# Performance work log

Hardware: AMD Instinct MI355X
Metric: run time of the kernel (lower is better)

## Reference

```python
import jax, jax.numpy as jnp
import numpy as np

L, B, CIN, H, W = 32, 4, 3, 16, 16
D, HEADS, DK, DEPTH = 64, 4, 16, 2
EPS = 1e-5
BN_INV = float(1.0 / np.sqrt(1.0 + EPS))  # eval-mode BatchNorm with default stats/affine


def conv2d(x, w, b=None, pad=1, groups=1):
    y = jax.lax.conv_general_dilated(
        x, w, window_strides=(1, 1), padding=[(pad, pad), (pad, pad)],
        dimension_numbers=('NCHW', 'OIHW', 'NCHW'), feature_group_count=groups)
    if b is not None:
        y = y + b[None, :, None, None]
    return y


def layer_norm(x, w, b):
    # LayerNorm over last 3 dims [D,H,W] of (L,B,D,H,W)
    mu = jnp.mean(x, axis=(-3, -2, -1), keepdims=True)
    var = jnp.var(x, axis=(-3, -2, -1), keepdims=True)
    return (x - mu) * jax.lax.rsqrt(var + EPS) * w + b


def pos_table():
    pos = jnp.arange(L, dtype=jnp.float32)
    exp = (2.0 * (jnp.arange(D) // 2).astype(jnp.float32)) / D
    angle = pos[:, None] / jnp.power(10000.0, exp)[None, :]  # (L, D)
    # source applies sin to even POSITIONS and cos to odd POSITIONS (table[0::2]=sin)
    tab = jnp.where((jnp.arange(L) % 2 == 0)[:, None], jnp.sin(angle), jnp.cos(angle))
    return tab[:, None, :, None, None]  # (L,1,D,1,1) broadcast over B,H,W


def reference(x, gw1, gb1, gw2, gb2, gw3, gb3, gw4, gb4,
              conv1_w, conv1_b, conv2_w, conv2_b, wq, wk, wv, w0,
              ln1_w, ln1_b, ln2_w, ln2_b, ff_w1, ff_b1, ff_w2, ff_b2):
    lrelu = lambda v: jax.nn.leaky_relu(v, 0.01)
    h = x.reshape(L * B, CIN, H, W)
    for w_, b_ in ((gw1, gb1), (gw2, gb2), (gw3, gb3), (gw4, gb4)):
        h = lrelu(conv2d(h, w_, b_) * BN_INV)
    xlb = h.reshape(L, B, D, H, W) + pos_table()

    for i in range(DEPTH):
        # ---- multi-head conv attention (dec=True) ----
        y = layer_norm(xlb, ln1_w[i], ln1_b[i])
        xa = jnp.transpose(y, (1, 2, 3, 4, 0))  # (B,D,H,W,L)
        # conv1 is a 1x1 conv == pointwise linear over channels, per head
        qkv = jnp.einsum('bchwl,noc->bnohwl', xa, conv1_w[i]) \
            + conv1_b[i][None, :, :, None, None, None]  # (B,HEADS,3D,H,W,L)
        q, k, v = jnp.split(qkv, 3, axis=2)  # each (B,HEADS,D,H,W,L)
        q = jnp.einsum('bnchwl,nck->bnkhwl', q, wq[i])  # (B,HEADS,DK,H,W,L)
        k = jnp.einsum('bnchwl,nck->bnkhwl', k, wk[i])
        v = jnp.einsum('bnchwl,nck->bnkhwl', v, wv[i])

        def head_conv(t):
            # 5x5 conv per head (no bias): conv2(Q_i + K_j) = conv_w(Q)_i + conv_w(K)_j + bias
            z = jnp.transpose(t, (0, 5, 1, 2, 3, 4)).reshape(B * L, HEADS * DK, H, W)
            z = conv2d(z, conv2_w[i].reshape(HEADS * DK, DK, 5, 5), None, pad=2, groups=HEADS)
            return jnp.transpose(z.reshape(B, L, HEADS, DK, H, W), (0, 2, 3, 4, 5, 1))

        cq = head_conv(q)
        ck = head_conv(k)
        logits = cq[..., :, None] + ck[..., None, :] \
            + conv2_b[i][None, :, :, None, None, None, None]  # (B,HEADS,DK,H,W,Lq,Lk)
        a = jax.nn.softmax(logits, axis=-1)
        vout = jnp.einsum('bnkhwij,bnkhwj->bnkhwi', a, v)   # (B,HEADS,DK,H,W,L)
        vcat = vout.reshape(B, D, H, W, L)                  # concat heads on channel dim
        attn = jnp.einsum('bchwl,co->bohwl', vcat, w0[i])
        xlb = xlb + jnp.transpose(attn, (4, 0, 1, 2, 3))

        # ---- feed-forward over the TIME dimension (Linear on L) ----
        y = layer_norm(xlb, ln2_w[i], ln2_b[i])
        xp = jnp.transpose(y, (1, 2, 3, 4, 0))  # (B,D,H,W,L)
        h1 = lrelu(jnp.einsum('bchwl,ml->bchwm', xp, ff_w1[i]) + ff_b1[i])
        ff = jnp.einsum('bchwm,lm->bchwl', h1, ff_w2[i]) + ff_b2[i]
        xlb = xlb + jnp.transpose(ff, (4, 0, 1, 2, 3))
    return xlb


def setup_inputs() -> dict:
    key = jax.random.key(0)
    specs = {
        'x': (L, B, CIN, H, W),
        'gw1': (4, 3, 3, 3), 'gb1': (4,), 'gw2': (6, 4, 3, 3), 'gb2': (6,),
        'gw3': (8, 6, 3, 3), 'gb3': (8,), 'gw4': (64, 8, 3, 3), 'gb4': (64,),
        'conv1_w': (DEPTH, HEADS, 3 * D, D), 'conv1_b': (DEPTH, HEADS, 3 * D),
        'conv2_w': (DEPTH, HEADS, DK, DK, 5, 5), 'conv2_b': (DEPTH, HEADS, DK),
        'wq': (DEPTH, HEADS, D, DK), 'wk': (DEPTH, HEADS, D, DK), 'wv': (DEPTH, HEADS, D, DK),
        'w0': (DEPTH, D, D),
        'ln1_w': (DEPTH, D, H, W), 'ln1_b': (DEPTH, D, H, W),
        'ln2_w': (DEPTH, D, H, W), 'ln2_b': (DEPTH, D, H, W),
        'ff_w1': (DEPTH, 4 * L, L), 'ff_b1': (DEPTH, 4 * L),
        'ff_w2': (DEPTH, L, 4 * L), 'ff_b2': (DEPTH, L),
    }
    out = {}
    for idx, (name, shape) in enumerate(specs.items()):
        g = jax.random.normal(jax.random.fold_in(key, idx), shape, dtype=jnp.float32)
        if name == 'x':
            out[name] = g
        elif name in ('ln1_w', 'ln2_w'):
            out[name] = 1.0 + 0.05 * g
        else:
            out[name] = 0.05 * g
    return out
```

## Files before the change

### kernel.cpp

```cpp
#include <hip/hip_runtime.h>
#include <math.h>

#define LL 32
#define BB 4
#define DD 64
#define NH 4
#define DKK 16
#define BN_INV 0.9999950000374997f

__device__ __forceinline__ float lrelu(float v){ return v > 0.f ? v : 0.01f*v; }

__global__ void k_eff(const float* __restrict__ c1w, const float* __restrict__ c1b,
                      const float* __restrict__ wk, const float* __restrict__ wv,
                      float* __restrict__ A, float* __restrict__ bf){
  int tid = blockIdx.x*256 + threadIdx.x;
  int k = tid & 15, d = (tid>>4)&63, n=(tid>>10)&3, t=(tid>>12)&1, i=tid>>13;
  const float* wsel = (t ? wv : wk) + (i*NH+n)*64*16;
  const float* cw   = c1w + ((i*NH+n)*192 + (t+1)*64)*64;
  float acc = 0.f;
  for(int c=0;c<64;++c) acc += cw[c*64+d]*wsel[c*16+k];
  A[tid] = acc;
  if(d==0){
    const float* cb = c1b + (i*NH+n)*192 + (t+1)*64;
    float ba=0.f;
    for(int c=0;c<64;++c) ba += cb[c]*wsel[c*16+k];
    bf[((i*2+t)*4+n)*16+k] = ba;
  }
}

__global__ void k_pos(float* __restrict__ pos){
  int tid = blockIdx.x*256 + threadIdx.x;
  int d = tid & 63, l = tid >> 6;
  float ex = (float)(d>>1) / 32.0f;
  float angle = (float)l * powf(10000.0f, -ex);
  pos[tid] = (l & 1) ? cosf(angle) : sinf(angle);
}

__global__ void k_wT(const float* __restrict__ w2, float* __restrict__ wT){
  int tid = blockIdx.x*256 + threadIdx.x;
  int k = tid & 15; int rest = tid >> 4;
  int tap = rest % 25; int rest2 = rest / 25;
  int c = rest2 & 15; int dn = rest2 >> 4;
  wT[tid] = w2[((dn*16 + k)*16 + c)*25 + tap];
}

__global__ void k_wT3(const float* __restrict__ gw4, float* __restrict__ wT3){
  int tid = blockIdx.x*256 + threadIdx.x;
  if(tid >= 4608) return;
  int co = tid & 63, ct = tid >> 6;
  wT3[ct*64 + co] = gw4[co*72 + ct];
}

__global__ void k_w2T(const float* __restrict__ w2, float* __restrict__ w2T){
  int tid = blockIdx.x*256 + threadIdx.x;
  int l = tid & 31; int m = (tid>>5)&127; int dep = tid>>12;
  w2T[tid] = w2[dep*4096 + l*128 + m];
}

__global__ __launch_bounds__(256) void k_front(const float* __restrict__ x,
    const float* __restrict__ gw1, const float* __restrict__ gb1,
    const float* __restrict__ gw2, const float* __restrict__ gb2,
    const float* __restrict__ gw3, const float* __restrict__ gb3,
    float* __restrict__ out8){
  __shared__ float sh[4212];
  float* T0 = sh; float* T1 = sh + 972; float* T2 = sh + 2268;
  int f = blockIdx.x, t = threadIdx.x;
  int h = t>>4, w = t&15;
  for(int j=t;j<4212;j+=256) sh[j]=0.f;
  __syncthreads();
  for(int ci=0;ci<3;++ci) T0[ci*324 + (h+1)*18 + (w+1)] = x[f*768 + ci*256 + t];
  __syncthreads();
  for(int co=0;co<4;++co){
    float acc = gb1[co];
    for(int ci=0;ci<3;++ci){
      const float* tb = T0 + ci*324 + h*18 + w;
      const float* wb = gw1 + co*27 + ci*9;
      #pragma unroll
      for(int dy=0;dy<3;++dy)
        #pragma unroll
        for(int dx=0;dx<3;++dx) acc += tb[dy*18+dx]*wb[dy*3+dx];
    }
    T1[co*324 + (h+1)*18 + (w+1)] = lrelu(acc*BN_INV);
  }
  __syncthreads();
  for(int co=0;co<6;++co){
    float acc = gb2[co];
    for(int ci=0;ci<4;++ci){
      const float* tb = T1 + ci*324 + h*18 + w;
      const float* wb = gw2 + co*36 + ci*9;
      #pragma unroll
      for(int dy=0;dy<3;++dy)
        #pragma unroll
        for(int dx=0;dx<3;++dx) acc += tb[dy*18+dx]*wb[dy*3+dx];
    }
    T2[co*324 + (h+1)*18 + (w+1)] = lrelu(acc*BN_INV);
  }
  __syncthreads();
  for(int co=0;co<8;++co){
    float acc = gb3[co];
    for(int ci=0;ci<6;++ci){
      const float* tb = T2 + ci*324 + h*18 + w;
      const float* wb = gw3 + co*54 + ci*9;
      #pragma unroll
      for(int dy=0;dy<3;++dy)
        #pragma unroll
        for(int dx=0;dx<3;++dx) acc += tb[dy*18+dx]*wb[dy*3+dx];
    }
    out8[f*2048 + co*256 + t] = lrelu(acc*BN_INV);
  }
}

__global__ __launch_bounds__(256) void k_conv3_l4(const float* __restrict__ in8,
    const float* __restrict__ wT3, const float* __restrict__ gb4,
    const float* __restrict__ pos, float* __restrict__ out){
  __shared__ float tile[8*324];
  __shared__ float wsl[1152];
  int blk = blockIdx.x; int g = blk & 3; int f = blk >> 2;
  int t = threadIdx.x; int h = t>>4, w = t&15;
  for(int j=t;j<2592;j+=256) tile[j]=0.f;
  for(int j=t;j<1152;j+=256){
    int ct = j>>4, c16 = j&15;
    wsl[j] = wT3[ct*64 + g*16 + c16];
  }
  __syncthreads();
  for(int ci=0;ci<8;++ci) tile[ci*324 + (h+1)*18 + (w+1)] = in8[f*2048 + ci*256 + t];
  __syncthreads();
  float acc[16];
  #pragma unroll
  for(int q=0;q<16;++q) acc[q] = gb4[g*16+q];
  for(int ci=0;ci<8;++ci){
    const float* tb = tile + ci*324 + h*18 + w;
    #pragma unroll
    for(int dy=0;dy<3;++dy){
      #pragma unroll
      for(int dx=0;dx<3;++dx){
        float v = tb[dy*18+dx];
        const float* wp = wsl + (ci*9+dy*3+dx)*16;
        float4 wa = *(const float4*)(wp);
        float4 wb = *(const float4*)(wp+4);
        float4 wc = *(const float4*)(wp+8);
        float4 wd = *(const float4*)(wp+12);
        acc[0]+=v*wa.x; acc[1]+=v*wa.y; acc[2]+=v*wa.z; acc[3]+=v*wa.w;
        acc[4]+=v*wb.x; acc[5]+=v*wb.y; acc[6]+=v*wb.z; acc[7]+=v*wb.w;
        acc[8]+=v*wc.x; acc[9]+=v*wc.y; acc[10]+=v*wc.z; acc[11]+=v*wc.w;
        acc[12]+=v*wd.x; acc[13]+=v*wd.y; acc[14]+=v*wd.z; acc[15]+=v*wd.w;
      }
    }
  }
  int l = f >> 2;
  #pragma unroll
  for(int q=0;q<16;++q){
    float r = lrelu(acc[q]*BN_INV) + pos[l*64 + g*16 + q];
    out[f*16384 + (g*16+q)*256 + t] = r;
  }
}

__global__ __launch_bounds__(1024) void k_ln(const float* __restrict__ x,
                     const float* __restrict__ w, const float* __restrict__ b,
                     float* __restrict__ y){
  int g = blockIdx.x, t = threadIdx.x;
  const float4* xb = (const float4*)(x + g*16384);
  float4 xv[4];
  float s=0.f, s2=0.f;
  #pragma unroll
  for(int j=0;j<4;++j){
    float4 v = xb[t + j*1024];
    xv[j] = v;
    s  += v.x + v.y + v.z + v.w;
    s2 += v.x*v.x + v.y*v.y + v.z*v.z + v.w*v.w;
  }
  __shared__ float ls[1024], ls2[1024];
  ls[t]=s; ls2[t]=s2; __syncthreads();
  for(int off=512;off>0;off>>=1){
    if(t<off){ ls[t]+=ls[t+off]; ls2[t]+=ls2[t+off]; }
    __syncthreads();
  }
  float mu  = ls[0]*(1.0f/16384.f);
  float var = ls2[0]*(1.0f/16384.f) - mu*mu;
  float rinv = rsqrtf(var + 1e-5f);
  const float4* wb = (const float4*)w;
  const float4* bb = (const float4*)b;
  float4* yb = (float4*)(y + g*16384);
  #pragma unroll
  for(int j=0;j<4;++j){
    int e = t + j*1024;
    float4 v = xv[j], wv = wb[e], bv = bb[e], o;
    o.x = (v.x-mu)*rinv*wv.x + bv.x;
    o.y = (v.y-mu)*rinv*wv.y + bv.y;
    o.z = (v.z-mu)*rinv*wv.z + bv.z;
    o.w = (v.w-mu)*rinv*wv.w + bv.w;
    yb[e] = o;
  }
}

__global__ __launch_bounds__(256) void k_kv(const float* __restrict__ y,
                     const float* __restrict__ A, const float* __restrict__ bf,
                     float* __restrict__ K, float* __restrict__ V, int dep){
  int blk = blockIdx.x;
  int n = blk & 3; int lb = blk >> 2;
  int t = threadIdx.x;
  const float* yb  = y + lb*16384 + t;
  const float* akb = A + ((dep*2+0)*4+n)*1024;
  const float* avb = A + ((dep*2+1)*4+n)*1024;
  float kacc[16], vacc[16];
  #pragma unroll
  for(int q=0;q<16;++q){
    kacc[q] = bf[((dep*2+0)*4+n)*16+q];
    vacc[q] = bf[((dep*2+1)*4+n)*16+q];
  }
  for(int d=0;d<64;++d){
    float yv = yb[d*256];
    const float* ak = akb + d*16;
    const float* av = avb + d*16;
    #pragma unroll
    for(int q=0;q<16;++q){ kacc[q] += yv*ak[q]; vacc[q] += yv*av[q]; }
  }
  int l = lb >> 2, b = lb & 3;
  int base = ((b*32+l)*4+n)*4096 + t;
  #pragma unroll
  for(int q=0;q<16;++q){ K[base + q*256] = kacc[q]; V[base + q*256] = vacc[q]; }
}

__global__ __launch_bounds__(256) void k_conv5(const float* __restrict__ K,
                       const float* __restrict__ wT, float* __restrict__ CK, int dep){
  __shared__ float tile[16*400];
  int blk = blockIdx.x;
  int khalf = blk & 1; int fh = blk >> 1; int n = fh & 3;
  int t = threadIdx.x;
  const float* kb = K + fh*4096;
  for(int j=t;j<6400;j+=256) tile[j]=0.f;
  __syncthreads();
  int h = t>>4, w = t&15;
  for(int c=0;c<16;++c) tile[c*400 + (h+2)*20 + (w+2)] = kb[c*256+t];
  __syncthreads();
  const float* wb = wT + (dep*4+n)*6400 + khalf*8;
  float acc[8] = {0.f,0.f,0.f,0.f,0.f,0.f,0.f,0.f};
  for(int c=0;c<16;++c){
    const float* tb = tile + c*400 + h*20 + w;
    const float* wc = wb + c*400;
    #pragma unroll
    for(int dy=0;dy<5;++dy){
      #pragma unroll
      for(int dx=0;dx<5;++dx){
        float v = tb[dy*20+dx];
        const float* wp = wc + (dy*5+dx)*16;
        float4 wa = *(const float4*)(wp);
        float4 wbv = *(const float4*)(wp+4);
        acc[0]+=v*wa.x; acc[1]+=v*wa.y; acc[2]+=v*wa.z; acc[3]+=v*wa.w;
        acc[4]+=v*wbv.x; acc[5]+=v*wbv.y; acc[6]+=v*wbv.z; acc[7]+=v*wbv.w;
      }
    }
  }
  float* ob = CK + fh*4096 + khalf*8*256;
  #pragma unroll
  for(int q=0;q<8;++q) ob[q*256+t] = acc[q];
}

__global__ void k_soft(const float* __restrict__ CK, const float* __restrict__ V,
                       float* __restrict__ vout){
  int idx = blockIdx.x*256 + threadIdx.x;
  int p = idx&255; int k=(idx>>8)&15; int n=(idx>>12)&3; int b=idx>>14;
  int base = (b*128 + n)*4096 + k*256 + p;
  float e[32]; float m = -1e30f;
  for(int l=0;l<32;++l){ float v = CK[base + l*16384]; e[l]=v; m = fmaxf(m,v); }
  float s = 0.f;
  for(int l=0;l<32;++l){ e[l] = expf(e[l]-m); s += e[l]; }
  float inv = 1.f/s, acc = 0.f;
  for(int l=0;l<32;++l) acc += e[l]*V[base + l*16384];
  vout[((b*4+n)*16+k)*256+p] = acc*inv;
}

__global__ void k_w0res(const float* __restrict__ vout, const float* __restrict__ w0,
                        float* __restrict__ xlb, int dep){
  int idx = blockIdx.x*256 + threadIdx.x;
  int p = idx&255; int o=(idx>>8)&63; int b=idx>>14;
  const float* vb = vout + b*64*256 + p;
  const float* wb = w0 + dep*4096 + o;
  float acc = 0.f;
  for(int c=0;c<64;++c) acc += vb[c*256]*wb[c*64];
  for(int l=0;l<32;++l) xlb[((l*4+b)*64+o)*256 + p] += acc;
}

__global__ __launch_bounds__(256) void k_ff(const float* __restrict__ y,
                     const float* __restrict__ w1, const float* __restrict__ b1,
                     const float* __restrict__ w2T, const float* __restrict__ b2,
                     float* __restrict__ xlb, int dep){
  __shared__ float pfa[4*2048];
  int t = threadIdx.x;
  int lane = t & 63;
  int w = __builtin_amdgcn_readfirstlane(t >> 6);
  int blk = blockIdx.x;
  int elem = blk*64 + lane;
  float yv[32];
  #pragma unroll
  for(int l=0;l<32;++l) yv[l] = y[elem + l*65536];
  float fa[32];
  if(w==0){
    #pragma unroll
    for(int l=0;l<32;++l) fa[l] = b2[dep*32+l];
  } else {
    #pragma unroll
    for(int l=0;l<32;++l) fa[l] = 0.f;
  }
  const float* w1b  = w1  + dep*4096 + w*1024;
  const float* w2Tb = w2T + dep*4096 + w*1024;
  const float* b1b  = b1  + dep*128  + w*32;
  #pragma unroll 4
  for(int mm=0;mm<32;++mm){
    float s0=0.f,s1=0.f,s2=0.f,s3=0.f;
    #pragma unroll
    for(int l=0;l<32;l+=4){
      s0 += yv[l+0]*w1b[mm*32+l+0];
      s1 += yv[l+1]*w1b[mm*32+l+1];
      s2 += yv[l+2]*w1b[mm*32+l+2];
      s3 += yv[l+3]*w1b[mm*32+l+3];
    }
    float s = lrelu(((s0+s1)+(s2+s3)) + b1b[mm]);
    #pragma unroll
    for(int l=0;l<32;++l) fa[l] += s*w2Tb[mm*32+l];
  }
  #pragma unroll
  for(int l=0;l<32;++l) pfa[w*2048 + l*64 + lane] = fa[l];
  __syncthreads();
  #pragma unroll
  for(int j=0;j<8;++j){
    int pi = t + j*256;
    float sum = pfa[pi] + pfa[pi+2048] + pfa[pi+4096] + pfa[pi+6144];
    int l = pi >> 6, ln2 = pi & 63;
    xlb[blk*64 + ln2 + l*65536] += sum;
  }
}

extern "C" void kernel_launch(void* const* d_in, const int* in_sizes, int n_in,
                              void* d_out, int out_size, void* d_ws, size_t ws_size,
                              hipStream_t stream) {
  const float* x       = (const float*)d_in[0];
  const float* gw1     = (const float*)d_in[1];
  const float* gb1     = (const float*)d_in[2];
  const float* gw2     = (const float*)d_in[3];
  const float* gb2     = (const float*)d_in[4];
  const float* gw3     = (const float*)d_in[5];
  const float* gb3     = (const float*)d_in[6];
  const float* gw4     = (const float*)d_in[7];
  const float* gb4     = (const float*)d_in[8];
  const float* conv1_w = (const float*)d_in[9];
  const float* conv1_b = (const float*)d_in[10];
  const float* conv2_w = (const float*)d_in[11];
  const float* wk      = (const float*)d_in[14];
  const float* wv      = (const float*)d_in[15];
  const float* w0      = (const float*)d_in[16];
  const float* ln1_w   = (const float*)d_in[17];
  const float* ln1_b   = (const float*)d_in[18];
  const float* ln2_w   = (const float*)d_in[19];
  const float* ln2_b   = (const float*)d_in[20];
  const float* ff_w1   = (const float*)d_in[21];
  const float* ff_b1   = (const float*)d_in[22];
  const float* ff_w2   = (const float*)d_in[23];
  const float* ff_b2   = (const float*)d_in[24];

  float* out = (float*)d_out;
  float* ws  = (float*)d_ws;
  float* Y    = ws;
  float* K    = ws + 2097152;
  float* CK   = ws + 4194304;
  float* V    = ws + 6291456;
  float* vout = ws + 8388608;
  float* A    = ws + 8454144;
  float* bf   = ws + 8470528;
  float* pos  = ws + 8470784;
  float* wT   = ws + 8472832;
  float* wT3  = ws + 8524032;
  float* w2T  = ws + 8528640;

  k_eff<<<64, 256, 0, stream>>>(conv1_w, conv1_b, wk, wv, A, bf);
  k_pos<<<8, 256, 0, stream>>>(pos);
  k_wT <<<200, 256, 0, stream>>>(conv2_w, wT);
  k_wT3<<<18, 256, 0, stream>>>(gw4, wT3);
  k_w2T<<<32, 256, 0, stream>>>(ff_w2, w2T);

  k_front   <<<128, 256, 0, stream>>>(x, gw1, gb1, gw2, gb2, gw3, gb3, K);
  k_conv3_l4<<<512, 256, 0, stream>>>(K, wT3, gb4, pos, out);

  for(int dep=0; dep<2; ++dep){
    k_ln   <<<128, 1024, 0, stream>>>(out, ln1_w + dep*16384, ln1_b + dep*16384, Y);
    k_kv   <<<512,  256, 0, stream>>>(Y, A, bf, K, V, dep);
    k_conv5<<<1024, 256, 0, stream>>>(K, wT, CK, dep);
    k_soft <<<256,  256, 0, stream>>>(CK, V, vout);
    k_w0res<<<256,  256, 0, stream>>>(vout, w0, out, dep);
    k_ln   <<<128, 1024, 0, stream>>>(out, ln2_w + dep*16384, ln2_b + dep*16384, Y);
    k_ff   <<<1024, 256, 0, stream>>>(Y, ff_w1, ff_b1, w2T, ff_b2, out, dep);
  }
}
```

Measured before the change: 326.3 us.

## Fuse LayerNorm apply into consumers and merge weight-prep kernels

Replaces the LayerNorm kernel, which wrote a full normalized tensor Y, with a stats-only kernel that stores mean and inverse std per frame. The normalization is then applied on the fly inside k_kv and k_ff, and k_ff reuses its loaded x values for the residual instead of re-reading and accumulating. The five small weight-prep kernels are merged into one launch. This removes a full write and read of Y per LayerNorm and several launches, at the cost of redundant normalization arithmetic: k_kv recomputes it across the 4 heads, and k_ff recomputes it across its 4 waves.

```diff
diff --git a/kernel.cpp b/kernel.cpp
--- a/kernel.cpp
+++ b/kernel.cpp
@@ -10,51 +10,49 @@
 
 __device__ __forceinline__ float lrelu(float v){ return v > 0.f ? v : 0.01f*v; }
 
-__global__ void k_eff(const float* __restrict__ c1w, const float* __restrict__ c1b,
-                      const float* __restrict__ wk, const float* __restrict__ wv,
-                      float* __restrict__ A, float* __restrict__ bf){
-  int tid = blockIdx.x*256 + threadIdx.x;
-  int k = tid & 15, d = (tid>>4)&63, n=(tid>>10)&3, t=(tid>>12)&1, i=tid>>13;
-  const float* wsel = (t ? wv : wk) + (i*NH+n)*64*16;
-  const float* cw   = c1w + ((i*NH+n)*192 + (t+1)*64)*64;
-  float acc = 0.f;
-  for(int c=0;c<64;++c) acc += cw[c*64+d]*wsel[c*16+k];
-  A[tid] = acc;
-  if(d==0){
-    const float* cb = c1b + (i*NH+n)*192 + (t+1)*64;
-    float ba=0.f;
-    for(int c=0;c<64;++c) ba += cb[c]*wsel[c*16+k];
-    bf[((i*2+t)*4+n)*16+k] = ba;
-  }
-}
-
-__global__ void k_pos(float* __restrict__ pos){
-  int tid = blockIdx.x*256 + threadIdx.x;
-  int d = tid & 63, l = tid >> 6;
-  float ex = (float)(d>>1) / 32.0f;
-  float angle = (float)l * powf(10000.0f, -ex);
-  pos[tid] = (l & 1) ? cosf(angle) : sinf(angle);
-}
-
-__global__ void k_wT(const float* __restrict__ w2, float* __restrict__ wT){
-  int tid = blockIdx.x*256 + threadIdx.x;
-  int k = tid & 15; int rest = tid >> 4;
-  int tap = rest % 25; int rest2 = rest / 25;
-  int c = rest2 & 15; int dn = rest2 >> 4;
-  wT[tid] = w2[((dn*16 + k)*16 + c)*25 + tap];
-}
-
-__global__ void k_wT3(const float* __restrict__ gw4, float* __restrict__ wT3){
-  int tid = blockIdx.x*256 + threadIdx.x;
-  if(tid >= 4608) return;
-  int co = tid & 63, ct = tid >> 6;
-  wT3[ct*64 + co] = gw4[co*72 + ct];
-}
-
-__global__ void k_w2T(const float* __restrict__ w2, float* __restrict__ w2T){
-  int tid = blockIdx.x*256 + threadIdx.x;
-  int l = tid & 31; int m = (tid>>5)&127; int dep = tid>>12;
-  w2T[tid] = w2[dep*4096 + l*128 + m];
+__global__ __launch_bounds__(256) void k_prep(
+    const float* __restrict__ c1w, const float* __restrict__ c1b,
+    const float* __restrict__ wk,  const float* __restrict__ wv,
+    const float* __restrict__ w2,  const float* __restrict__ gw4,
+    const float* __restrict__ ffw2,
+    float* __restrict__ A, float* __restrict__ bf, float* __restrict__ pos,
+    float* __restrict__ wT, float* __restrict__ wT3, float* __restrict__ w2T){
+  int blk = blockIdx.x, t = threadIdx.x;
+  if(blk < 64){
+    int tid = blk*256 + t;
+    int k = tid & 15, d = (tid>>4)&63, n=(tid>>10)&3, tt=(tid>>12)&1, i=tid>>13;
+    const float* wsel = (tt ? wv : wk) + (i*NH+n)*64*16;
+    const float* cw   = c1w + ((i*NH+n)*192 + (tt+1)*64)*64;
+    float acc = 0.f;
+    for(int c=0;c<64;++c) acc += cw[c*64+d]*wsel[c*16+k];
+    A[tid] = acc;
+    if(d==0){
+      const float* cb = c1b + (i*NH+n)*192 + (tt+1)*64;
+      float ba=0.f;
+      for(int c=0;c<64;++c) ba += cb[c]*wsel[c*16+k];
+      bf[((i*2+tt)*4+n)*16+k] = ba;
+    }
+  } else if(blk < 72){
+    int tid = (blk-64)*256 + t;
+    int d = tid & 63, l = tid >> 6;
+    float ex = (float)(d>>1) / 32.0f;
+    float angle = (float)l * powf(10000.0f, -ex);
+    pos[tid] = (l & 1) ? cosf(angle) : sinf(angle);
+  } else if(blk < 272){
+    int tid = (blk-72)*256 + t;
+    int k = tid & 15; int rest = tid >> 4;
+    int tap = rest % 25; int rest2 = rest / 25;
+    int c = rest2 & 15; int dn = rest2 >> 4;
+    wT[tid] = w2[((dn*16 + k)*16 + c)*25 + tap];
+  } else if(blk < 290){
+    int tid = (blk-272)*256 + t;
+    int co = tid & 63, ct = tid >> 6;
+    wT3[ct*64 + co] = gw4[co*72 + ct];
+  } else {
+    int tid = (blk-290)*256 + t;
+    int l = tid & 31; int m = (tid>>5)&127; int dep = tid>>12;
+    w2T[tid] = ffw2[dep*4096 + l*128 + m];
+  }
 }
 
 __global__ __launch_bounds__(256) void k_front(const float* __restrict__ x,
@@ -155,17 +153,14 @@
   }
 }
 
-__global__ __launch_bounds__(1024) void k_ln(const float* __restrict__ x,
-                     const float* __restrict__ w, const float* __restrict__ b,
-                     float* __restrict__ y){
+__global__ __launch_bounds__(1024) void k_stats(const float* __restrict__ x,
+                                                float* __restrict__ stats){
   int g = blockIdx.x, t = threadIdx.x;
   const float4* xb = (const float4*)(x + g*16384);
-  float4 xv[4];
   float s=0.f, s2=0.f;
   #pragma unroll
   for(int j=0;j<4;++j){
     float4 v = xb[t + j*1024];
-    xv[j] = v;
     s  += v.x + v.y + v.z + v.w;
     s2 += v.x*v.x + v.y*v.y + v.z*v.z + v.w*v.w;
   }
@@ -175,31 +170,26 @@
     if(t<off){ ls[t]+=ls[t+off]; ls2[t]+=ls2[t+off]; }
     __syncthreads();
   }
-  float mu  = ls[0]*(1.0f/16384.f);
-  float var = ls2[0]*(1.0f/16384.f) - mu*mu;
-  float rinv = rsqrtf(var + 1e-5f);
-  const float4* wb = (const float4*)w;
-  const float4* bb = (const float4*)b;
-  float4* yb = (float4*)(y + g*16384);
-  #pragma unroll
-  for(int j=0;j<4;++j){
-    int e = t + j*1024;
-    float4 v = xv[j], wv = wb[e], bv = bb[e], o;
-    o.x = (v.x-mu)*rinv*wv.x + bv.x;
-    o.y = (v.y-mu)*rinv*wv.y + bv.y;
-    o.z = (v.z-mu)*rinv*wv.z + bv.z;
-    o.w = (v.w-mu)*rinv*wv.w + bv.w;
-    yb[e] = o;
-  }
-}
-
-__global__ __launch_bounds__(256) void k_kv(const float* __restrict__ y,
+  if(t==0){
+    float mu  = ls[0]*(1.0f/16384.f);
+    float var = ls2[0]*(1.0f/16384.f) - mu*mu;
+    stats[g*2]   = mu;
+    stats[g*2+1] = rsqrtf(var + 1e-5f);
+  }
+}
+
+__global__ __launch_bounds__(256) void k_kv(const float* __restrict__ x,
+                     const float* __restrict__ lnw, const float* __restrict__ lnb,
+                     const float* __restrict__ stats,
                      const float* __restrict__ A, const float* __restrict__ bf,
                      float* __restrict__ K, float* __restrict__ V, int dep){
   int blk = blockIdx.x;
   int n = blk & 3; int lb = blk >> 2;
   int t = threadIdx.x;
-  const float* yb  = y + lb*16384 + t;
+  float mu = stats[lb*2], ri = stats[lb*2+1];
+  const float* xb  = x   + lb*16384 + t;
+  const float* wbp = lnw + t;
+  const float* bbp = lnb + t;
   const float* akb = A + ((dep*2+0)*4+n)*1024;
   const float* avb = A + ((dep*2+1)*4+n)*1024;
   float kacc[16], vacc[16];
@@ -209,7 +199,7 @@
     vacc[q] = bf[((dep*2+1)*4+n)*16+q];
   }
   for(int d=0;d<64;++d){
-    float yv = yb[d*256];
+    float yv = (xb[d*256]-mu)*ri*wbp[d*256] + bbp[d*256];
     const float* ak = akb + d*16;
     const float* av = avb + d*16;
     #pragma unroll
@@ -281,19 +271,31 @@
   for(int l=0;l<32;++l) xlb[((l*4+b)*64+o)*256 + p] += acc;
 }
 
-__global__ __launch_bounds__(256) void k_ff(const float* __restrict__ y,
+__global__ __launch_bounds__(256) void k_ff(float* __restrict__ xlb,
+                     const float* __restrict__ lnw, const float* __restrict__ lnb,
+                     const float* __restrict__ stats,
                      const float* __restrict__ w1, const float* __restrict__ b1,
                      const float* __restrict__ w2T, const float* __restrict__ b2,
-                     float* __restrict__ xlb, int dep){
+                     int dep){
   __shared__ float pfa[4*2048];
   int t = threadIdx.x;
   int lane = t & 63;
   int w = __builtin_amdgcn_readfirstlane(t >> 6);
   int blk = blockIdx.x;
   int elem = blk*64 + lane;
-  float yv[32];
-  #pragma unroll
-  for(int l=0;l<32;++l) yv[l] = y[elem + l*65536];
+  int b = elem >> 14;
+  int e = elem & 16383;
+  float lw  = lnw[e];
+  float lbv = lnb[e];
+  float xv[32], yv[32];
+  #pragma unroll
+  for(int l=0;l<32;++l) xv[l] = xlb[elem + l*65536];
+  #pragma unroll
+  for(int l=0;l<32;++l){
+    float mu = stats[(l*4+b)*2];
+    float ri = stats[(l*4+b)*2+1];
+    yv[l] = (xv[l]-mu)*ri*lw + lbv;
+  }
   float fa[32];
   if(w==0){
     #pragma unroll
@@ -326,8 +328,8 @@
   for(int j=0;j<8;++j){
     int pi = t + j*256;
     float sum = pfa[pi] + pfa[pi+2048] + pfa[pi+4096] + pfa[pi+6144];
-    int l = pi >> 6, ln2 = pi & 63;
-    xlb[blk*64 + ln2 + l*65536] += sum;
+    int l = pi >> 6;
+    xlb[blk*64 + lane + l*65536] = xv[l] + sum;
   }
 }
 
@@ -360,34 +362,33 @@
 
   float* out = (float*)d_out;
   float* ws  = (float*)d_ws;
-  float* Y    = ws;
-  float* K    = ws + 2097152;
-  float* CK   = ws + 4194304;
-  float* V    = ws + 6291456;
-  float* vout = ws + 8388608;
-  float* A    = ws + 8454144;
-  float* bf   = ws + 8470528;
-  float* pos  = ws + 8470784;
-  float* wT   = ws + 8472832;
-  float* wT3  = ws + 8524032;
-  float* w2T  = ws + 8528640;
-
-  k_eff<<<64, 256, 0, stream>>>(conv1_w, conv1_b, wk, wv, A, bf);
-  k_pos<<<8, 256, 0, stream>>>(pos);
-  k_wT <<<200, 256, 0, stream>>>(conv2_w, wT);
-  k_wT3<<<18, 256, 0, stream>>>(gw4, wT3);
-  k_w2T<<<32, 256, 0, stream>>>(ff_w2, w2T);
+  float* K     = ws;
+  float* CK    = ws + 2097152;
+  float* V     = ws + 4194304;
+  float* vout  = ws + 6291456;
+  float* A     = ws + 6356992;
+  float* bf    = ws + 6373376;
+  float* pos   = ws + 6373632;
+  float* wT    = ws + 6375680;
+  float* wT3   = ws + 6426880;
+  float* w2T   = ws + 6431488;
+  float* stats = ws + 6439680;
+
+  k_prep<<<322, 256, 0, stream>>>(conv1_w, conv1_b, wk, wv, conv2_w, gw4, ff_w2,
+                                  A, bf, pos, wT, wT3, w2T);
 
   k_front   <<<128, 256, 0, stream>>>(x, gw1, gb1, gw2, gb2, gw3, gb3, K);
   k_conv3_l4<<<512, 256, 0, stream>>>(K, wT3, gb4, pos, out);
 
   for(int dep=0; dep<2; ++dep){
-    k_ln   <<<128, 1024, 0, stream>>>(out, ln1_w + dep*16384, ln1_b + dep*16384, Y);
-    k_kv   <<<512,  256, 0, stream>>>(Y, A, bf, K, V, dep);
+    k_stats<<<128, 1024, 0, stream>>>(out, stats);
+    k_kv   <<<512,  256, 0, stream>>>(out, ln1_w + dep*16384, ln1_b + dep*16384,
+                                      stats, A, bf, K, V, dep);
     k_conv5<<<1024, 256, 0, stream>>>(K, wT, CK, dep);
     k_soft <<<256,  256, 0, stream>>>(CK, V, vout);
     k_w0res<<<256,  256, 0, stream>>>(vout, w0, out, dep);
-    k_ln   <<<128, 1024, 0, stream>>>(out, ln2_w + dep*16384, ln2_b + dep*16384, Y);
-    k_ff   <<<1024, 256, 0, stream>>>(Y, ff_w1, ff_b1, w2T, ff_b2, out, dep);
-  }
-}
+    k_stats<<<128, 1024, 0, stream>>>(out, stats);
+    k_ff   <<<1024, 256, 0, stream>>>(out, ln2_w + dep*16384, ln2_b + dep*16384,
+                                      stats, ff_w1, ff_b1, w2T, ff_b2, dep);
+  }
+}
```

After: 319.2 us. -2.2%, faster.
